# Performance work log

Measured on AMD Instinct MI355X. Metric: run time of the kernel, lower is better.

Reference implementation:

```python
import math
import jax, jax.numpy as jnp
import numpy as np
from jax import lax

B, C, H, W, D = 8, 3, 512, 512, 256
KS, SIGMA = 13, 2.0  # GaussianBlur(13); torchvision samples sigma in (0.1,5.0) -> fixed for determinism


def tanh01(v):
    return jnp.tanh(v) * 0.5 + 0.5


def tanh_range(v, left, right):
    return tanh01(v) * (right - left) + left


def norm01(v):
    return (v - v.min()) / (v.max() - v.min())


def gaussian_blur(x):
    r = KS // 2
    t = jnp.arange(KS, dtype=x.dtype) - r
    k = jnp.exp(-(t ** 2) / (2.0 * SIGMA ** 2))
    k = k / k.sum()
    b, c, h, w = x.shape
    xp = jnp.pad(x, ((0, 0), (0, 0), (r, r), (r, r)), mode='reflect').reshape(b * c, 1, h + 2 * r, w + 2 * r)
    y = lax.conv_general_dilated(xp, k.reshape(1, 1, KS, 1), (1, 1), 'VALID')
    y = lax.conv_general_dilated(y, k.reshape(1, 1, 1, KS), (1, 1), 'VALID')
    return y.reshape(b, c, h, w)


def dark_channel(x):
    return x.min(axis=1, keepdims=True)


def atmospheric_light(x, dark, top_k=1000):
    b, _, h, w = x.shape
    imsz = h * w
    numpx = max(imsz // top_k, 1)
    darkvec = dark.reshape(b, imsz)
    imvec = x.reshape(b, 3, imsz).transpose(0, 2, 1)  # [b, imsz, 3]
    idx = jnp.argsort(darkvec, axis=1)[:, imsz - numpx:]  # brightest dark-channel pixels
    gathered = jnp.take_along_axis(imvec, idx[:, :, None], axis=1)  # [b, numpx, 3]
    a = gathered[:, 1:, :].sum(axis=1) / numpx  # original loop skips index 0 of the slice
    return a[:, :, None, None]  # [b,3,1,1]


def fft_filter(x, rate, fft_gate):
    # rate: [b,1]; replicate torch.fft.fftshift default (shifts ALL axes, incl. batch/channel)
    b, c, w, h = x.shape  # note: original names w,h = shape[-2:]
    line = jnp.floor(jnp.sqrt(w * h * rate) / 2.0).astype(jnp.int32).reshape(-1)  # [b]
    rows = jnp.arange(w)
    cols = jnp.arange(h)
    mr = (rows[None, :] >= w // 2 - line[:, None]) & (rows[None, :] < w // 2 + line[:, None])
    mc = (cols[None, :] >= h // 2 - line[:, None]) & (cols[None, :] < h // 2 + line[:, None])
    mask = (mr[:, None, :, None] & mc[:, None, None, :]).astype(x.dtype)  # [b,1,w,h]
    mask = jnp.broadcast_to(mask, x.shape)
    F = jnp.fft.fftshift(jnp.fft.fft2(x, norm='forward'))
    F = F * (1.0 - mask)
    inv = jnp.fft.ifft2(jnp.fft.ifftshift(F), norm='forward').real
    return jnp.abs(inv) * fft_gate[:, None, None, None]


def setup_inputs() -> dict:
    key = jax.random.key(0)
    ks = jax.random.split(key, 20)
    def lin_w(k, i, o):
        return (jax.random.normal(k, (i, o)) * 0.02).astype(jnp.float32)
    def lin_b(k, o):
        return (jax.random.normal(k, (o,)) * 0.02).astype(jnp.float32)
    return {
        'x': jax.random.uniform(ks[0], (B, C, H, W), dtype=jnp.float32),
        'latent': (jax.random.normal(ks[1], (B, D)) * 0.5).astype(jnp.float32),
        'gate_w': lin_w(ks[2], D, 8), 'gate_b': lin_b(ks[3], 8),
        'wb_w': lin_w(ks[4], D, 3), 'wb_b': lin_b(ks[5], 3),
        'gamma_w': lin_w(ks[6], D, 1), 'gamma_b': lin_b(ks[7], 1),
        'sharp_w': lin_w(ks[8], D, 1), 'sharp_b': lin_b(ks[9], 1),
        'defog_w': lin_w(ks[10], D, 1), 'defog_b': lin_b(ks[11], 1),
        'contrast_w': lin_w(ks[12], D, 1), 'contrast_b': lin_b(ks[13], 1),
        'tone_w': lin_w(ks[14], D, 8), 'tone_b': lin_b(ks[15], 8),
        'fft_w': lin_w(ks[16], D, 1), 'fft_b': lin_b(ks[17], 1),
    }


def reference(x, latent, gate_w, gate_b, wb_w, wb_b, gamma_w, gamma_b, sharp_w, sharp_b,
              defog_w, defog_b, contrast_w, contrast_b, tone_w, tone_b, fft_w, fft_b):
    gate = tanh_range(latent @ gate_w + gate_b, 0.01, 1.0)  # [B,8]

    # white balance
    wb = jnp.exp(tanh_range(latent @ wb_w + wb_b, -0.5, 0.5))
    cs = 1.0 / (1e-5 + 0.27 * wb[:, 0] + 0.67 * wb[:, 1] + 0.06 * wb[:, 2])
    wb = cs[:, None] * wb
    wb_out = norm01(wb[:, :, None, None] * x) * gate[:, 0][:, None, None, None]

    # gamma balance
    lg = math.log(2.5)
    gamma = jnp.exp(tanh_range(latent @ gamma_w + gamma_b, -lg, lg))[:, :, None, None]
    g_out = norm01(jnp.maximum(x, 1e-4) ** gamma) * gate[:, 1][:, None, None, None]

    # identity
    id_out = x * gate[:, 2][:, None, None, None]

    # sharpening
    y = tanh_range(latent @ sharp_w + sharp_b, 0.1, 1.0)[:, :, None, None]
    s = x + y * (x - gaussian_blur(x))
    sharp_out = norm01(s) * gate[:, 3][:, None, None, None]

    # defog (atmospheric scattering model)
    omega = tanh_range(latent @ defog_w + defog_b, 0.1, 1.0)[:, :, None, None]
    dark = dark_channel(x)
    a = atmospheric_light(x, dark)
    t = 1.0 - omega * dark_channel(x / a)
    j = (x - a) / jnp.maximum(t, 0.01) + a
    fog_out = norm01(j) * gate[:, 4][:, None, None, None]

    # contrast
    alpha = jnp.tanh(latent @ contrast_w + contrast_b)[:, :, None, None]
    lum = jnp.clip(0.27 * x[:, 0] + 0.67 * x[:, 1] + 0.06 * x[:, 2], 0.0, 1.0)[:, None]
    clum = -jnp.cos(math.pi * lum) * 0.5 + 0.5
    cimg = x / (lum + 1e-6) * clum
    cimg = (1.0 - alpha) * x + alpha * cimg
    contrast_out = norm01(cimg) * gate[:, 5][:, None, None, None]

    # tone curve (8 fixed segments)
    tc = tanh_range(latent @ tone_w + tone_b, 0.5, 2.0)  # [B,8]
    tsum = tc.sum(axis=1) + 1e-30
    total = jnp.zeros_like(x)
    for i in range(8):
        total = total + jnp.clip(x - i / 8.0, 0.0, 1.0 / 8.0) * tc[:, i][:, None, None, None]
    total = total * (8.0 / tsum)[:, None, None, None]
    tone_out = norm01(total) * gate[:, 6][:, None, None, None]

    # fft frequency masking
    rate = tanh_range(latent @ fft_w + fft_b, 0.1, 0.8)  # [B,1]
    fft_out = fft_filter(x, rate, gate[:, 7])

    return norm01(wb_out + g_out + id_out + sharp_out + fog_out + contrast_out + tone_out + fft_out)
```

## Files before the change

kernel.cpp:

```cpp
#include <hip/hip_runtime.h>
#include <math.h>

#define HW 262144
#define TOTAL 6291456
#define PI_F 3.14159265358979323846f
#define NBIN 1024
#define PIDX(i) ((i) + ((i) >> 3))


#define PF_GATE 0
#define PF_WB 64
#define PF_GAMMA 88
#define PF_Y 96
#define PF_OMEGA 104
#define PF_ALPHA 112
#define PF_TC 120
#define PF_TSC 184
#define PF_RATE 192
#define PF_FG 200
#define PF_A 208
#define PF_WBM 256
#define PF_WBA 264
#define PF_GM 272
#define PF_GA 280
#define PF_SM 288
#define PF_SA 296
#define PF_FM 304
#define PF_FA 312
#define PF_CM 320
#define PF_CA 328
#define PF_TM 336
#define PF_TA 344
#define PF_LINE 360

#define QX(b,c) ((b)*3+(c))
#define QS 24
#define QJ 25
#define QC 26
#define QFIN 27
#define SL_LCOUNT 1792
#define SL_BINSTAR 1920
#define SL_RNEED 1928
#define SL_SUMA2 2048

struct GK { float w[13]; };

__device__ __forceinline__ unsigned fkey(float f){
    unsigned u = __float_as_uint(f);
    return (u & 0x80000000u) ? ~u : (u | 0x80000000u);
}
__device__ __forceinline__ float funkey(unsigned k){
    return (k & 0x80000000u) ? __uint_as_float(k & 0x7FFFFFFFu) : __uint_as_float(~k);
}

__device__ __forceinline__ void blockRedPair(unsigned kmn, unsigned kmx, int q,
                                             unsigned* slots, unsigned* lds8){
    #pragma unroll
    for (int o = 32; o > 0; o >>= 1){
        kmn = min(kmn, __shfl_down(kmn, o));
        kmx = max(kmx, __shfl_down(kmx, o));
    }
    int w = threadIdx.x >> 6;
    if ((threadIdx.x & 63) == 0){ lds8[w] = kmn; lds8[4+w] = kmx; }
    __syncthreads();
    if (threadIdx.x == 0){
        unsigned mn = min(min(lds8[0],lds8[1]), min(lds8[2],lds8[3]));
        unsigned mx = max(max(lds8[4],lds8[5]), max(lds8[6],lds8[7]));
        int s = blockIdx.x & 31;
        atomicMin(&slots[q*64 + s], mn);
        atomicMax(&slots[q*64 + 32 + s], mx);
    }
    __syncthreads();
}

__device__ __forceinline__ float toneF(float v, const float* tc, float tsc){
    float tn = 0.f;
    #pragma unroll
    for (int i = 0; i < 8; ++i){
        float d = v - 0.125f * (float)i;
        d = fminf(fmaxf(d, 0.f), 0.125f);
        tn += d * tc[i];
    }
    return tn * tsc;
}

__device__ __forceinline__ float2 cadd(float2 a, float2 b){ return make_float2(a.x+b.x, a.y+b.y); }
__device__ __forceinline__ float2 csub(float2 a, float2 b){ return make_float2(a.x-b.x, a.y-b.y); }
__device__ __forceinline__ float2 cmul(float2 a, float2 b){ return make_float2(a.x*b.x - a.y*b.y, a.x*b.y + a.y*b.x); }

template<int S>
__device__ __forceinline__ float2 rot90(float2 z){
    return (S < 0) ? make_float2(z.y, -z.x) : make_float2(-z.y, z.x);
}

template<int S>
__device__ __forceinline__ void fft4p(float2 a, float2 b, float2 c, float2 d,
                                      float2& X0, float2& X1, float2& X2, float2& X3){
    float2 t0 = cadd(a,c), t1 = csub(a,c), t2 = cadd(b,d), t3 = csub(b,d);
    float2 it3 = rot90<S>(t3);
    X0 = cadd(t0,t2); X2 = csub(t0,t2);
    X1 = cadd(t1,it3); X3 = csub(t1,it3);
}

template<int S>
__device__ __forceinline__ void bfly8(float2 v[8]){
    const float C = 0.70710678118654752f;
    float2 E0,E1,E2,E3,O0,O1,O2,O3;
    fft4p<S>(v[0],v[2],v[4],v[6], E0,E1,E2,E3);
    fft4p<S>(v[1],v[3],v[5],v[7], O0,O1,O2,O3);
    float2 w1 = make_float2(C, (S<0) ? -C : C);
    float2 w3 = make_float2(-C, (S<0) ? -C : C);
    float2 u1 = cmul(O1, w1);
    float2 u2 = rot90<S>(O2);
    float2 u3 = cmul(O3, w3);
    v[0]=cadd(E0,O0); v[4]=csub(E0,O0);
    v[1]=cadd(E1,u1); v[5]=csub(E1,u1);
    v[2]=cadd(E2,u2); v[6]=csub(E2,u2);
    v[3]=cadd(E3,u3); v[7]=csub(E3,u3);
}

__device__ __forceinline__ void twiddles(float2 v[8], float th){
    float sn, cs; __sincosf(th, &sn, &cs);
    float2 w1 = make_float2(cs, sn);
    float2 w = w1;
    v[1] = cmul(v[1], w1);
    #pragma unroll
    for (int r = 2; r < 8; ++r){ w = cmul(w, w1); v[r] = cmul(v[r], w); }
}

template<int S>
__device__ __forceinline__ void fft512reg(float2 v[8], float2* buf, int lane){
    bfly8<S>(v);
    #pragma unroll
    for (int q = 0; q < 8; ++q) buf[PIDX(8*lane + q)] = v[q];
    __syncthreads();
    #pragma unroll
    for (int r = 0; r < 8; ++r) v[r] = buf[PIDX(lane + 64*r)];
    __syncthreads();
    twiddles(v, (float)S * 6.2831853072f * (float)(lane & 7) * (1.0f/64.0f));
    bfly8<S>(v);
    {
        int basei = ((lane >> 3) << 6) + (lane & 7);
        #pragma unroll
        for (int q = 0; q < 8; ++q) buf[PIDX(basei + 8*q)] = v[q];
    }
    __syncthreads();
    #pragma unroll
    for (int r = 0; r < 8; ++r) v[r] = buf[PIDX(lane + 64*r)];
    twiddles(v, (float)S * 6.2831853072f * (float)lane * (1.0f/512.0f));
    bfly8<S>(v);
}

__global__ __launch_bounds__(256) void kSetup(
    const float* __restrict__ lat,
    const float* gw, const float* gb, const float* wbw, const float* wbb,
    const float* gaw, const float* gab, const float* shw, const float* shb,
    const float* dfw, const float* dfb, const float* ctw, const float* ctb,
    const float* tow, const float* tob, const float* ffw, const float* ffb,
    float* P, unsigned* slots, unsigned* hist)
{
    if (blockIdx.x != 0){
        int i = (blockIdx.x - 1) * 256 + threadIdx.x;
        if (i < 4096) slots[i] = (i < 1792 && (i & 63) < 32) ? 0xFFFFFFFFu : 0u;
        if (i < 8192) hist[i] = 0u;
        return;
    }
    int t = threadIdx.x;
    if (t < 192){
        int b = t / 24, o = t % 24;
        const float* L = lat + b * 256;
        const float* W; float bias; int nc, col;
        if (o < 8)      { W=gw;  bias=gb[o];     nc=8; col=o;    }
        else if (o < 11){ W=wbw; bias=wbb[o-8];  nc=3; col=o-8;  }
        else if (o==11) { W=gaw; bias=gab[0];    nc=1; col=0;    }
        else if (o==12) { W=shw; bias=shb[0];    nc=1; col=0;    }
        else if (o==13) { W=dfw; bias=dfb[0];    nc=1; col=0;    }
        else if (o==14) { W=ctw; bias=ctb[0];    nc=1; col=0;    }
        else if (o<23)  { W=tow; bias=tob[o-15]; nc=8; col=o-15; }
        else            { W=ffw; bias=ffb[0];    nc=1; col=0;    }
        float acc = bias;
        for (int d = 0; d < 256; ++d) acc += L[d] * W[d*nc + col];
        float t01 = tanhf(acc) * 0.5f + 0.5f;
        if (o < 8){ float v = t01*0.99f + 0.01f; P[PF_GATE + b*8 + o] = v; if (o==7) P[PF_FG + b] = v; }
        else if (o < 11){ P[PF_WB + b*3 + (o-8)] = expf(t01 - 0.5f); }
        else if (o==11){ float lg = logf(2.5f); P[PF_GAMMA + b] = expf(t01*(2.f*lg) - lg); }
        else if (o==12){ P[PF_Y + b] = t01*0.9f + 0.1f; }
        else if (o==13){ P[PF_OMEGA + b] = t01*0.9f + 0.1f; }
        else if (o==14){ P[PF_ALPHA + b] = tanhf(acc); }
        else if (o<23){ P[PF_TC + b*8 + (o-15)] = t01*1.5f + 0.5f; }
        else { P[PF_RATE + b] = t01*0.7f + 0.1f; }
    }
    __syncthreads();
    if (t < 8){
        int b = t;
        float w0=P[PF_WB+b*3], w1=P[PF_WB+b*3+1], w2=P[PF_WB+b*3+2];
        float cs = 1.0f / (1e-5f + 0.27f*w0 + 0.67f*w1 + 0.06f*w2);
        P[PF_WB+b*3] = cs*w0; P[PF_WB+b*3+1] = cs*w1; P[PF_WB+b*3+2] = cs*w2;
        float ts = 0.f;
        for (int i = 0; i < 8; ++i) ts += P[PF_TC + b*8 + i];
        P[PF_TSC + b] = 8.0f / (ts + 1e-30f);
        int bs = (b + 4) & 7;
        ((int*)(P + PF_LINE))[b] = (int)floorf(sqrtf(262144.0f * P[PF_RATE + bs]) * 0.5f);
    }
}

__global__ __launch_bounds__(256) void kMinmaxHist(const float* __restrict__ x, unsigned* slots, unsigned* hist){
    __shared__ unsigned h[NBIN];
    __shared__ unsigned lds8[8];
    int b = blockIdx.x >> 7;
    int blk = blockIdx.x & 127;
    for (int i = threadIdx.x; i < NBIN; i += 256) h[i] = 0u;
    __syncthreads();
    size_t xb = (size_t)b*3*HW;
    int p0 = (((blk<<1)    )*256 + threadIdx.x) << 2;
    int p1 = (((blk<<1) + 1)*256 + threadIdx.x) << 2;
    float4 u0 = *(const float4*)(x + xb + p0);
    float4 u1 = *(const float4*)(x + xb + HW + p0);
    float4 u2 = *(const float4*)(x + xb + 2*HW + p0);
    float4 w0 = *(const float4*)(x + xb + p1);
    float4 w1 = *(const float4*)(x + xb + HW + p1);
    float4 w2 = *(const float4*)(x + xb + 2*HW + p1);
    float a0[8] = {u0.x,u0.y,u0.z,u0.w, w0.x,w0.y,w0.z,w0.w};
    float a1[8] = {u1.x,u1.y,u1.z,u1.w, w1.x,w1.y,w1.z,w1.w};
    float a2[8] = {u2.x,u2.y,u2.z,u2.w, w2.x,w2.y,w2.z,w2.w};
    float mn0=1e30f,mx0=-1e30f,mn1=1e30f,mx1=-1e30f,mn2=1e30f,mx2=-1e30f;
    #pragma unroll
    for (int e = 0; e < 8; ++e){
        float dark = fminf(a0[e], fminf(a1[e], a2[e]));
        atomicAdd(&h[min(NBIN-1, (int)(dark * (float)NBIN))], 1u);
        mn0 = fminf(mn0, a0[e]); mx0 = fmaxf(mx0, a0[e]);
        mn1 = fminf(mn1, a1[e]); mx1 = fmaxf(mx1, a1[e]);
        mn2 = fminf(mn2, a2[e]); mx2 = fmaxf(mx2, a2[e]);
    }
    __syncthreads();
    for (int i = threadIdx.x; i < NBIN; i += 256){
        unsigned c = h[i];
        if (c) atomicAdd(&hist[b*NBIN + i], c);
    }
    blockRedPair(fkey(mn0), fkey(mx0), QX(b,0), slots, lds8);
    blockRedPair(fkey(mn1), fkey(mx1), QX(b,1), slots, lds8);
    blockRedPair(fkey(mn2), fkey(mx2), QX(b,2), slots, lds8);
}

__global__ __launch_bounds__(256) void kScanHist(const unsigned* __restrict__ hist, unsigned* slots){
    int b = blockIdx.x, t = threadIdx.x;
    __shared__ unsigned wtot[4];
    __shared__ int doneS;
    if (t == 0) doneS = 0;
    __syncthreads();
    unsigned total = 0;
    for (int c0 = 0; c0 < NBIN; c0 += 256){
        int binIdx = NBIN-1 - (c0 + t);
        unsigned cnt = hist[b*NBIN + binIdx];
        unsigned v = cnt;
        #pragma unroll
        for (int off = 1; off < 64; off <<= 1){
            unsigned u = __shfl_up(v, off);
            if ((t & 63) >= off) v += u;
        }
        if ((t & 63) == 63) wtot[t >> 6] = v;
        __syncthreads();
        unsigned wofs = 0;
        for (int w = 0; w < (t >> 6); ++w) wofs += wtot[w];
        unsigned incl = total + wofs + v;
        unsigned excl = incl - cnt;
        if (incl >= 261u && excl < 261u){
            slots[SL_BINSTAR + b] = (unsigned)binIdx;
            slots[SL_RNEED + b]   = 261u - excl;
            doneS = 1;
        }
        __syncthreads();
        if (doneS) break;
        total += wtot[0] + wtot[1] + wtot[2] + wtot[3];
        __syncthreads();
    }
}

__global__ __launch_bounds__(256) void kCollect(const float* __restrict__ x, unsigned* slots, uint2* list){
    __shared__ float wsum[3][4];
    int b = blockIdx.x >> 8;
    int tile = blockIdx.x & 255;
    size_t xb = (size_t)b*3*HW;
    int p = (tile*256 + threadIdx.x) << 2;
    float4 v0 = *(const float4*)(x + xb + p);
    float4 v1 = *(const float4*)(x + xb + HW + p);
    float4 v2 = *(const float4*)(x + xb + 2*HW + p);
    int bs = (int)slots[SL_BINSTAR + b];
    float a0[4] = {v0.x,v0.y,v0.z,v0.w};
    float a1[4] = {v1.x,v1.y,v1.z,v1.w};
    float a2[4] = {v2.x,v2.y,v2.z,v2.w};
    float s0 = 0.f, s1 = 0.f, s2 = 0.f;
    #pragma unroll
    for (int e = 0; e < 4; ++e){
        float dark = fminf(a0[e], fminf(a1[e], a2[e]));
        int bin = min(NBIN-1, (int)(dark * (float)NBIN));
        if (bin > bs){ s0 += a0[e]; s1 += a1[e]; s2 += a2[e]; }
        else if (bin == bs){
            unsigned n = atomicAdd(&slots[SL_LCOUNT + b], 1u);
            if (n < 1024u) list[(b << 10) + n] = make_uint2(__float_as_uint(dark), (unsigned)(p + e));
        }
    }
    #pragma unroll
    for (int o = 32; o > 0; o >>= 1){
        s0 += __shfl_down(s0, o); s1 += __shfl_down(s1, o); s2 += __shfl_down(s2, o);
    }
    int w = threadIdx.x >> 6;
    if ((threadIdx.x & 63) == 0){ wsum[0][w] = s0; wsum[1][w] = s1; wsum[2][w] = s2; }
    __syncthreads();
    if (threadIdx.x == 0){
        float t0 = wsum[0][0]+wsum[0][1]+wsum[0][2]+wsum[0][3];
        float t1 = wsum[1][0]+wsum[1][1]+wsum[1][2]+wsum[1][3];
        float t2 = wsum[2][0]+wsum[2][1]+wsum[2][2]+wsum[2][3];
        float* F = (float*)(slots + SL_SUMA2);
        int sl = blockIdx.x & 31;
        atomicAdd(&F[(b*3+0)*32 + sl], t0);
        atomicAdd(&F[(b*3+1)*32 + sl], t1);
        atomicAdd(&F[(b*3+2)*32 + sl], t2);
    }
}

__global__ void kSelect(const float* __restrict__ x, uint2* list, unsigned* slots, float* P){
    __shared__ unsigned pid[262];
    __shared__ char taken[1024];
    int b = blockIdx.x, t = threadIdx.x;
    int n = (int)min(slots[SL_LCOUNT + b], 1024u);
    int r = (int)slots[SL_RNEED + b];
    if (r > n) r = n;
    const uint2* L = &list[b << 10];
    for (int i = t; i < n; i += 64) taken[i] = 0;
    __syncthreads();
    for (int it = 0; it < r; ++it){
        unsigned long long bk = 0ull; int bp = -1;
        for (int i = t; i < n; i += 64){
            if (taken[i]) continue;
            uint2 e = L[i];
            unsigned long long key = ((unsigned long long)e.x << 32) | e.y;
            if (key > bk){ bk = key; bp = i; }
        }
        #pragma unroll
        for (int o = 32; o > 0; o >>= 1){
            unsigned long long ok = __shfl_down(bk, o);
            int op = __shfl_down(bp, o);
            if (ok > bk){ bk = ok; bp = op; }
        }
        bp = __shfl(bp, 0);
        if (t == 0){ pid[it] = L[bp].y; taken[bp] = 1; }
        __syncthreads();
    }
    float s0 = 0.f, s1 = 0.f, s2 = 0.f;
    size_t xb = (size_t)b*3*HW;
    for (int i = t; i < r; i += 64){
        unsigned id = pid[i];
        s0 += x[xb + id]; s1 += x[xb + HW + id]; s2 += x[xb + 2*HW + id];
    }
    #pragma unroll
    for (int o = 32; o > 0; o >>= 1){
        s0 += __shfl_down(s0, o); s1 += __shfl_down(s1, o); s2 += __shfl_down(s2, o);
    }
    if (t == 0){
        const float* F = (const float*)(slots + SL_SUMA2);
        float f0 = 0.f, f1 = 0.f, f2 = 0.f;
        for (int k = 0; k < 32; ++k){
            f0 += F[(b*3+0)*32 + k];
            f1 += F[(b*3+1)*32 + k];
            f2 += F[(b*3+2)*32 + k];
        }
        P[PF_A + b*3+0] = (s0 + f0) / 262.0f;
        P[PF_A + b*3+1] = (s1 + f1) / 262.0f;
        P[PF_A + b*3+2] = (s2 + f2) / 262.0f;
    }
}

__global__ __launch_bounds__(256) void kBlur(const float* __restrict__ x, float* __restrict__ blurOut,
                                             const float* __restrict__ P, unsigned* slots, GK gk){
    __shared__ float tile[76][80];
    __shared__ float hbuf[76][68];
    __shared__ unsigned lds8[8];
    int img = blockIdx.x >> 6;
    int tid = blockIdx.x & 63;
    int tr0 = (tid >> 3) << 6;
    int tc0 = (tid & 7) << 6;
    size_t ib = (size_t)img * HW;
    int t = threadIdx.x;
    for (int l = t; l < 76*76; l += 256){
        int r = l / 76, c = l - r*76;
        int gr = tr0 + r - 6; gr = (gr < 0) ? -gr : ((gr > 511) ? 1022 - gr : gr);
        int gc = tc0 + c - 6; gc = (gc < 0) ? -gc : ((gc > 511) ? 1022 - gc : gc);
        tile[r][c] = x[ib + ((size_t)gr << 9) + gc];
    }
    __syncthreads();
    for (int l = t; l < 76*64; l += 256){
        int r = l >> 6, c = l & 63;
        float acc = 0.f;
        #pragma unroll
        for (int k = 0; k < 13; ++k) acc += gk.w[k] * tile[r][c + k];
        hbuf[r][c] = acc;
    }
    __syncthreads();
    float yb = P[PF_Y + img/3];
    unsigned kmn = 0xFFFFFFFFu, kmx = 0u;
    for (int l = t; l < 64*64; l += 256){
        int r = l >> 6, c = l & 63;
        float acc = 0.f;
        #pragma unroll
        for (int k = 0; k < 13; ++k) acc += gk.w[k] * hbuf[r + k][c];
        blurOut[ib + ((size_t)(tr0 + r) << 9) + tc0 + c] = acc;
        float xv = tile[r + 6][c + 6];
        float s = xv + yb * (xv - acc);
        unsigned key = fkey(s);
        kmn = min(kmn, key); kmx = max(kmx, key);
    }
    blockRedPair(kmn, kmx, QS, slots, lds8);
}

__global__ __launch_bounds__(256) void kFftRowFwdJC(const float* __restrict__ x, float2* __restrict__ bc,
                                                    const float* __restrict__ P, unsigned* slots){
    __shared__ float xs[3][512];
    __shared__ float2 buf[3][580];
    __shared__ unsigned lds8[8];
    int b = blockIdx.x >> 9;
    int row = blockIdx.x & 511;
    int t = threadIdx.x;
    size_t rowoff = ((size_t)row << 9);
    #pragma unroll
    for (int ch = 0; ch < 3; ++ch){
        float2 z = *(const float2*)(x + (size_t)(3*b + ch)*HW + rowoff + 2*t);
        xs[ch][2*t] = z.x; xs[ch][2*t+1] = z.y;
    }
    __syncthreads();
    {
        float a0 = P[PF_A+b*3], a1 = P[PF_A+b*3+1], a2 = P[PF_A+b*3+2];
        float om = P[PF_OMEGA+b], al = P[PF_ALPHA+b];
        float jmn = 1e30f, jmx = -1e30f, cmn = 1e30f, cmx = -1e30f;
        #pragma unroll
        for (int e = 0; e < 2; ++e){
            int i = 2*t + e;
            float x0 = xs[0][i], x1 = xs[1][i], x2 = xs[2][i];
            float dr = fminf(x0/a0, fminf(x1/a1, x2/a2));
            float T = fmaxf(1.0f - om*dr, 0.01f);
            float j0 = (x0-a0)/T + a0, j1 = (x1-a1)/T + a1, j2 = (x2-a2)/T + a2;
            float lum = fminf(fmaxf(0.27f*x0 + 0.67f*x1 + 0.06f*x2, 0.f), 1.f);
            float clum = -__cosf(PI_F*lum)*0.5f + 0.5f;
            float il = clum / (lum + 1e-6f);
            float c0 = (1.f-al)*x0 + al*(x0*il);
            float c1 = (1.f-al)*x1 + al*(x1*il);
            float c2 = (1.f-al)*x2 + al*(x2*il);
            jmn = fminf(jmn, fminf(j0, fminf(j1, j2))); jmx = fmaxf(jmx, fmaxf(j0, fmaxf(j1, j2)));
            cmn = fminf(cmn, fminf(c0, fminf(c1, c2))); cmx = fmaxf(cmx, fmaxf(c0, fmaxf(c1, c2)));
        }
        blockRedPair(fkey(jmn), fkey(jmx), QJ, slots, lds8);
        blockRedPair(fkey(cmn), fkey(cmx), QC, slots, lds8);
    }
    bool act = t < 192;
    int ch = t >> 6, lane = t & 63;
    float2 v[8];
    if (act){
        #pragma unroll
        for (int r = 0; r < 8; ++r) v[r] = make_float2(xs[ch][lane + 64*r] * (1.0f/512.0f), 0.f);
        bfly8<-1>(v);
        #pragma unroll
        for (int q = 0; q < 8; ++q) buf[ch][PIDX(8*lane + q)] = v[q];
    }
    __syncthreads();
    if (act){
        #pragma unroll
        for (int r = 0; r < 8; ++r) v[r] = buf[ch][PIDX(lane + 64*r)];
    }
    __syncthreads();
    if (act){
        twiddles(v, -6.2831853072f * (float)(lane & 7) * (1.0f/64.0f));
        bfly8<-1>(v);
        int basei = ((lane >> 3) << 6) + (lane & 7);
        #pragma unroll
        for (int q = 0; q < 8; ++q) buf[ch][PIDX(basei + 8*q)] = v[q];
    }
    __syncthreads();
    if (act){
        #pragma unroll
        for (int r = 0; r < 8; ++r) v[r] = buf[ch][PIDX(lane + 64*r)];
        twiddles(v, -6.2831853072f * (float)lane * (1.0f/512.0f));
        bfly8<-1>(v);
        size_t ib = (size_t)(3*b + ch)*HW + rowoff;
        #pragma unroll
        for (int q = 0; q < 8; ++q) bc[ib + lane + 64*q] = v[q];
    }
}

__global__ __launch_bounds__(256) void kFftColMid(float2* __restrict__ bc, const int* __restrict__ lineS){
    int img  = blockIdx.x >> 6;
    int tile = blockIdx.x & 63;
    int c0 = tile << 3;
    int line = lineS[img / 3];
    if (c0 >= line && c0 + 8 <= 512 - line) return;
    __shared__ float2 cb[8][580];
    int t = threadIdx.x;
    size_t ibase = (size_t)img*HW + c0;
    for (int k = 0; k < 16; ++k){
        int idx = (k << 8) + t;
        int row = idx >> 3, col = idx & 7;
        float2 z = bc[ibase + ((size_t)row << 9) + col];
        cb[col][PIDX(row)] = make_float2(z.x * (1.0f/512.0f), z.y * (1.0f/512.0f));
    }
    __syncthreads();
    int lane = t & 63;
    #pragma unroll
    for (int h = 0; h < 2; ++h){
        int col = (h << 2) + (t >> 6);
        int cc = c0 + col;
        bool colM = (cc < line) || (cc >= 512 - line);
        float2 v[8];
        #pragma unroll
        for (int r = 0; r < 8; ++r) v[r] = cb[col][PIDX(lane + 64*r)];
        __syncthreads();
        fft512reg<-1>(v, cb[col], lane);
        if (colM){
            #pragma unroll
            for (int q = 0; q < 8; ++q){
                int f = lane + (q << 6);
                if (f < line || f >= 512 - line) v[q] = make_float2(0.f, 0.f);
            }
        }
        __syncthreads();
        fft512reg<+1>(v, cb[col], lane);
        __syncthreads();
        #pragma unroll
        for (int q = 0; q < 8; ++q) cb[col][PIDX(lane + 64*q)] = v[q];
        __syncthreads();
    }
    for (int k = 0; k < 16; ++k){
        int idx = (k << 8) + t;
        int row = idx >> 3, col = idx & 7;
        int cc = c0 + col;
        if (cc < line || cc >= 512 - line)
            bc[ibase + ((size_t)row << 9) + col] = cb[col][PIDX(row)];
    }
}

__global__ __launch_bounds__(256) void kCombineFFT(const float* __restrict__ x, float* __restrict__ outb,
                                                   const float2* __restrict__ bc, const float* __restrict__ P,
                                                   unsigned* slots){
    __shared__ float2 buf[3][580];
    __shared__ float fbuf[3][512];
    __shared__ unsigned lds8[8];
    int b = blockIdx.x >> 9;
    int row = blockIdx.x & 511;
    int t = threadIdx.x;
    bool act = t < 192;
    int ch = t >> 6, lane = t & 63;
    size_t rowoff = ((size_t)row << 9);
    float2 v[8];
    if (act){
        size_t ib = (size_t)(3*b + ch)*HW + rowoff;
        #pragma unroll
        for (int r = 0; r < 8; ++r) v[r] = bc[ib + lane + 64*r];
        bfly8<1>(v);
        #pragma unroll
        for (int q = 0; q < 8; ++q) buf[ch][PIDX(8*lane + q)] = v[q];
    }
    __syncthreads();
    if (act){
        #pragma unroll
        for (int r = 0; r < 8; ++r) v[r] = buf[ch][PIDX(lane + 64*r)];
    }
    __syncthreads();
    if (act){
        twiddles(v, 6.2831853072f * (float)(lane & 7) * (1.0f/64.0f));
        bfly8<1>(v);
        int basei = ((lane >> 3) << 6) + (lane & 7);
        #pragma unroll
        for (int q = 0; q < 8; ++q) buf[ch][PIDX(basei + 8*q)] = v[q];
    }
    __syncthreads();
    if (act){
        #pragma unroll
        for (int r = 0; r < 8; ++r) v[r] = buf[ch][PIDX(lane + 64*r)];
        twiddles(v, 6.2831853072f * (float)lane * (1.0f/512.0f));
        bfly8<1>(v);
        #pragma unroll
        for (int q = 0; q < 8; ++q) fbuf[ch][lane + 64*q] = fabsf(v[q].x);
    }
    __syncthreads();

    float g  = P[PF_FG + b];
    float wb0=P[PF_WB+b*3], wb1=P[PF_WB+b*3+1], wb2=P[PF_WB+b*3+2];
    float gam=P[PF_GAMMA+b], yb=P[PF_Y+b], om=P[PF_OMEGA+b], al=P[PF_ALPHA+b];
    float a0=P[PF_A+b*3], a1=P[PF_A+b*3+1], a2=P[PF_A+b*3+2];
    float g2=P[PF_GATE+b*8+2];
    float wbm=P[PF_WBM+b], wba=P[PF_WBA+b], gm=P[PF_GM+b], ga=P[PF_GA+b];
    float sm=P[PF_SM+b], sa=P[PF_SA+b], fm=P[PF_FM+b], fa=P[PF_FA+b];
    float cm=P[PF_CM+b], ca=P[PF_CA+b], tm=P[PF_TM+b], ta=P[PF_TA+b];
    float tc[8];
    #pragma unroll
    for (int i = 0; i < 8; ++i) tc[i] = P[PF_TC + b*8 + i];
    float tsc = P[PF_TSC+b];

    size_t p0 = (size_t)(3*b)*HW + rowoff + 2*t;
    float2 xv0 = *(const float2*)(x + p0);
    float2 xv1 = *(const float2*)(x + p0 + HW);
    float2 xv2 = *(const float2*)(x + p0 + 2*HW);
    float2 bv0 = *(const float2*)(outb + p0);
    float2 bv1 = *(const float2*)(outb + p0 + HW);
    float2 bv2 = *(const float2*)(outb + p0 + 2*HW);
    float X0[2] = {xv0.x, xv0.y}, X1[2] = {xv1.x, xv1.y}, X2[2] = {xv2.x, xv2.y};
    float B0[2] = {bv0.x, bv0.y}, B1[2] = {bv1.x, bv1.y}, B2[2] = {bv2.x, bv2.y};
    float O0[2], O1[2], O2[2];
    float mn = 1e30f, mx = -1e30f;
    #pragma unroll
    for (int e = 0; e < 2; ++e){
        int i = 2*t + e;
        float f0 = fbuf[0][i] * g;
        float f1 = fbuf[1][i] * g;
        float f2 = fbuf[2][i] * g;
        float x0 = X0[e], x1 = X1[e], x2 = X2[e];
        float dr = fminf(x0/a0, fminf(x1/a1, x2/a2));
        float T = fmaxf(1.0f - om*dr, 0.01f);
        float lum = fminf(fmaxf(0.27f*x0 + 0.67f*x1 + 0.06f*x2, 0.f), 1.f);
        float clum = -__cosf(PI_F*lum)*0.5f + 0.5f;
        float il = clum / (lum + 1e-6f);
        float s, j, ci, tn, gp;
        s = x0 + yb*(x0 - B0[e]); j = (x0 - a0)/T + a0; ci = (1.f-al)*x0 + al*(x0*il);
        tn = toneF(x0, tc, tsc); gp = __powf(fmaxf(x0, 1e-4f), gam);
        float sum0 = (wb0*x0)*wbm + wba + gp*gm + ga + x0*g2 + s*sm + sa + j*fm + fa + ci*cm + ca + tn*tm + ta + f0;
        s = x1 + yb*(x1 - B1[e]); j = (x1 - a1)/T + a1; ci = (1.f-al)*x1 + al*(x1*il);
        tn = toneF(x1, tc, tsc); gp = __powf(fmaxf(x1, 1e-4f), gam);
        float sum1 = (wb1*x1)*wbm + wba + gp*gm + ga + x1*g2 + s*sm + sa + j*fm + fa + ci*cm + ca + tn*tm + ta + f1;
        s = x2 + yb*(x2 - B2[e]); j = (x2 - a2)/T + a2; ci = (1.f-al)*x2 + al*(x2*il);
        tn = toneF(x2, tc, tsc); gp = __powf(fmaxf(x2, 1e-4f), gam);
        float sum2 = (wb2*x2)*wbm + wba + gp*gm + ga + x2*g2 + s*sm + sa + j*fm + fa + ci*cm + ca + tn*tm + ta + f2;
        O0[e] = sum0; O1[e] = sum1; O2[e] = sum2;
        mn = fminf(mn, fminf(sum0, fminf(sum1, sum2)));
        mx = fmaxf(mx, fmaxf(sum0, fmaxf(sum1, sum2)));
    }
    *(float2*)(outb + p0)        = make_float2(O0[0], O0[1]);
    *(float2*)(outb + p0 + HW)   = make_float2(O1[0], O1[1]);
    *(float2*)(outb + p0 + 2*HW) = make_float2(O2[0], O2[1]);
    blockRedPair(fkey(mn), fkey(mx), QFIN, slots, lds8);
}

__global__ void kNormParams(float* P, const unsigned* __restrict__ slots){
    __shared__ float mnv[28], mxv[28];
    int t = threadIdx.x;
    if (t < 28){
        unsigned kmn = 0xFFFFFFFFu, kmx = 0u;
        for (int s = 0; s < 32; ++s){
            kmn = min(kmn, slots[t*64 + s]);
            kmx = max(kmx, slots[t*64 + 32 + s]);
        }
        mnv[t] = funkey(kmn); mxv[t] = funkey(kmx);
    }
    __syncthreads();
    if (t == 0){
        float wmin=1e30f, wmax=-1e30f, gmin=1e30f, gmax=-1e30f, tmin=1e30f, tmax=-1e30f;
        for (int b = 0; b < 8; ++b){
            float gam = P[PF_GAMMA+b];
            float tsc = P[PF_TSC+b];
            const float* tc = &P[PF_TC + b*8];
            float xbmin = 1e30f, xbmax = -1e30f;
            for (int c = 0; c < 3; ++c){
                int i = b*3 + c;
                float w = P[PF_WB + i];
                wmin = fminf(wmin, w * mnv[i]); wmax = fmaxf(wmax, w * mxv[i]);
                gmin = fminf(gmin, __powf(fmaxf(mnv[i], 1e-4f), gam));
                gmax = fmaxf(gmax, __powf(fmaxf(mxv[i], 1e-4f), gam));
                xbmin = fminf(xbmin, mnv[i]); xbmax = fmaxf(xbmax, mxv[i]);
            }
            tmin = fminf(tmin, toneF(xbmin, tc, tsc));
            tmax = fmaxf(tmax, toneF(xbmax, tc, tsc));
        }
        float smin = mnv[QS], smax = mxv[QS];
        float jmin = mnv[QJ], jmax = mxv[QJ];
        float cmin = mnv[QC], cmax = mxv[QC];
        for (int b = 0; b < 8; ++b){
            const float* G = &P[PF_GATE + b*8];
            float m;
            m = G[0]/(wmax-wmin); P[PF_WBM+b]=m; P[PF_WBA+b]=-wmin*m;
            m = G[1]/(gmax-gmin); P[PF_GM +b]=m; P[PF_GA +b]=-gmin*m;
            m = G[3]/(smax-smin); P[PF_SM +b]=m; P[PF_SA +b]=-smin*m;
            m = G[4]/(jmax-jmin); P[PF_FM +b]=m; P[PF_FA +b]=-jmin*m;
            m = G[5]/(cmax-cmin); P[PF_CM +b]=m; P[PF_CA +b]=-cmin*m;
            m = G[6]/(tmax-tmin); P[PF_TM +b]=m; P[PF_TA +b]=-tmin*m;
        }
    }
}

__global__ __launch_bounds__(256) void kFinalNorm(float* __restrict__ out, const unsigned* __restrict__ slots){
    unsigned kmn = 0xFFFFFFFFu, kmx = 0u;
    for (int s = 0; s < 32; ++s){
        kmn = min(kmn, slots[QFIN*64 + s]);
        kmx = max(kmx, slots[QFIN*64 + 32 + s]);
    }
    float mn = funkey(kmn), mx = funkey(kmx);
    float inv = 1.0f / (mx - mn);
    size_t i = ((size_t)blockIdx.x*256 + threadIdx.x) << 2;
    float4 v = *(const float4*)(out + i);
    v.x = (v.x - mn) * inv; v.y = (v.y - mn) * inv;
    v.z = (v.z - mn) * inv; v.w = (v.w - mn) * inv;
    *(float4*)(out + i) = v;
}

extern "C" void kernel_launch(void* const* d_in, const int* in_sizes, int n_in,
                              void* d_out, int out_size, void* d_ws, size_t ws_size,
                              hipStream_t stream){
    const float* x   = (const float*)d_in[0];
    const float* lat = (const float*)d_in[1];
    const float* gw  = (const float*)d_in[2];  const float* gb  = (const float*)d_in[3];
    const float* wbw = (const float*)d_in[4];  const float* wbb = (const float*)d_in[5];
    const float* gaw = (const float*)d_in[6];  const float* gab = (const float*)d_in[7];
    const float* shw = (const float*)d_in[8];  const float* shb = (const float*)d_in[9];
    const float* dfw = (const float*)d_in[10]; const float* dfb = (const float*)d_in[11];
    const float* ctw = (const float*)d_in[12]; const float* ctb = (const float*)d_in[13];
    const float* tow = (const float*)d_in[14]; const float* tob = (const float*)d_in[15];
    const float* ffw = (const float*)d_in[16]; const float* ffb = (const float*)d_in[17];
    float* out = (float*)d_out;
    char* ws = (char*)d_ws;

    float*    P     = (float*)ws;
    unsigned* slots = (unsigned*)(ws + 2048);
    unsigned* hist  = (unsigned*)(ws + 20480);
    uint2*    list  = (uint2*)(ws + 540672);
    float2*   bufC  = (float2*)(ws + 1048576);
    const int* lineS = (const int*)(P + PF_LINE);

    GK gk;
    {
        float s = 0.f;
        for (int i = 0; i < 13; ++i){ float t = (float)i - 6.f; gk.w[i] = expf(-(t*t)/8.0f); s += gk.w[i]; }
        for (int i = 0; i < 13; ++i) gk.w[i] /= s;
    }

    hipLaunchKernelGGL(kSetup,       dim3(41),   dim3(256), 0, stream, lat, gw,gb,wbw,wbb,gaw,gab,shw,shb,dfw,dfb,ctw,ctb,tow,tob,ffw,ffb, P, slots, hist);
    hipLaunchKernelGGL(kMinmaxHist,  dim3(1024), dim3(256), 0, stream, x, slots, hist);
    hipLaunchKernelGGL(kScanHist,    dim3(8),    dim3(256), 0, stream, hist, slots);
    hipLaunchKernelGGL(kCollect,     dim3(2048), dim3(256), 0, stream, x, slots, list);
    hipLaunchKernelGGL(kSelect,      dim3(8),    dim3(64),  0, stream, x, list, slots, P);
    hipLaunchKernelGGL(kBlur,        dim3(1536), dim3(256), 0, stream, x, out, P, slots, gk);
    hipLaunchKernelGGL(kFftRowFwdJC, dim3(4096), dim3(256), 0, stream, x, bufC, P, slots);
    hipLaunchKernelGGL(kFftColMid,   dim3(1536), dim3(256), 0, stream, bufC, lineS);
    hipLaunchKernelGGL(kNormParams,  dim3(1),    dim3(64),  0, stream, P, slots);
    hipLaunchKernelGGL(kCombineFFT,  dim3(4096), dim3(256), 0, stream, x, out, bufC, P, slots);
    hipLaunchKernelGGL(kFinalNorm,   dim3(6144), dim3(256), 0, stream, out, slots);
}
```

Before: 236.7 us.

## Pack two real channels per complex FFT and process two rows per block

Channels R and G are packed into one complex signal (R + iG), and B goes into a second one. The row FFTs, the column pass and the inverse row FFTs then run on 2 complex images per batch instead of 3. Each block now handles two rows with all 256 threads active and float4 loads. Divisions by the atmospheric light are replaced with precomputed reciprocals, and the 8-segment tone curve becomes a single table lookup using precomputed prefix sums. Packing is only correct if the frequency mask is conjugate-symmetric, and the lookup changes floating-point rounding slightly.

```diff
diff --git a/kernel.cpp b/kernel.cpp
--- a/kernel.cpp
+++ b/kernel.cpp
@@ -32,6 +32,9 @@
 #define PF_TM 336
 #define PF_TA 344
 #define PF_LINE 360
+#define PF_TCS 368
+#define PF_TPRE 432
+#define PF_IA 496
 
 #define QX(b,c) ((b)*3+(c))
 #define QS 24
@@ -198,7 +201,15 @@
         P[PF_WB+b*3] = cs*w0; P[PF_WB+b*3+1] = cs*w1; P[PF_WB+b*3+2] = cs*w2;
         float ts = 0.f;
         for (int i = 0; i < 8; ++i) ts += P[PF_TC + b*8 + i];
-        P[PF_TSC + b] = 8.0f / (ts + 1e-30f);
+        float tsc = 8.0f / (ts + 1e-30f);
+        P[PF_TSC + b] = tsc;
+        float acc = 0.f;
+        for (int k = 0; k < 8; ++k){
+            float tck = P[PF_TC + b*8 + k] * tsc;
+            P[PF_TCS + b*8 + k] = tck;
+            P[PF_TPRE + b*8 + k] = acc;
+            acc += tck * 0.125f;
+        }
         int bs = (b + 4) & 7;
         ((int*)(P + PF_LINE))[b] = (int)floorf(sqrtf(262144.0f * P[PF_RATE + bs]) * 0.5f);
     }
@@ -365,9 +376,9 @@
             f1 += F[(b*3+1)*32 + k];
             f2 += F[(b*3+2)*32 + k];
         }
-        P[PF_A + b*3+0] = (s0 + f0) / 262.0f;
-        P[PF_A + b*3+1] = (s1 + f1) / 262.0f;
-        P[PF_A + b*3+2] = (s2 + f2) / 262.0f;
+        float A0 = (s0 + f0) / 262.0f, A1 = (s1 + f1) / 262.0f, A2 = (s2 + f2) / 262.0f;
+        P[PF_A + b*3+0] = A0; P[PF_A + b*3+1] = A1; P[PF_A + b*3+2] = A2;
+        P[PF_IA + b*3+0] = 1.0f/A0; P[PF_IA + b*3+1] = 1.0f/A1; P[PF_IA + b*3+2] = 1.0f/A2;
     }
 }
 
@@ -415,82 +426,69 @@
 
 __global__ __launch_bounds__(256) void kFftRowFwdJC(const float* __restrict__ x, float2* __restrict__ bc,
                                                     const float* __restrict__ P, unsigned* slots){
-    __shared__ float xs[3][512];
-    __shared__ float2 buf[3][580];
+    __shared__ float xs[2][3][512];
+    __shared__ float2 buf[4][580];
     __shared__ unsigned lds8[8];
-    int b = blockIdx.x >> 9;
-    int row = blockIdx.x & 511;
+    int b = blockIdx.x >> 8;
+    int rp = blockIdx.x & 255;
     int t = threadIdx.x;
-    size_t rowoff = ((size_t)row << 9);
-    #pragma unroll
-    for (int ch = 0; ch < 3; ++ch){
-        float2 z = *(const float2*)(x + (size_t)(3*b + ch)*HW + rowoff + 2*t);
-        xs[ch][2*t] = z.x; xs[ch][2*t+1] = z.y;
+    #pragma unroll
+    for (int k = 0; k < 3; ++k){
+        int l = t + (k << 8);
+        int seg = l >> 7;
+        int idx = (l & 127) << 2;
+        int ch = seg >> 1, rr = seg & 1;
+        float4 z = *(const float4*)(x + (size_t)(3*b + ch)*HW + ((size_t)(2*rp + rr) << 9) + idx);
+        *(float4*)&xs[rr][ch][idx] = z;
     }
     __syncthreads();
     {
-        float a0 = P[PF_A+b*3], a1 = P[PF_A+b*3+1], a2 = P[PF_A+b*3+2];
+        float ia0 = P[PF_IA+b*3], ia1 = P[PF_IA+b*3+1], ia2 = P[PF_IA+b*3+2];
+        float a0 = P[PF_A+b*3],  a1 = P[PF_A+b*3+1],  a2 = P[PF_A+b*3+2];
         float om = P[PF_OMEGA+b], al = P[PF_ALPHA+b];
+        int rr = t >> 7, c4 = (t & 127) << 2;
+        float4 xv0 = *(float4*)&xs[rr][0][c4];
+        float4 xv1 = *(float4*)&xs[rr][1][c4];
+        float4 xv2 = *(float4*)&xs[rr][2][c4];
+        float A0[4]={xv0.x,xv0.y,xv0.z,xv0.w}, A1[4]={xv1.x,xv1.y,xv1.z,xv1.w}, A2[4]={xv2.x,xv2.y,xv2.z,xv2.w};
         float jmn = 1e30f, jmx = -1e30f, cmn = 1e30f, cmx = -1e30f;
         #pragma unroll
-        for (int e = 0; e < 2; ++e){
-            int i = 2*t + e;
-            float x0 = xs[0][i], x1 = xs[1][i], x2 = xs[2][i];
-            float dr = fminf(x0/a0, fminf(x1/a1, x2/a2));
+        for (int e = 0; e < 4; ++e){
+            float x0 = A0[e], x1 = A1[e], x2 = A2[e];
+            float dr = fminf(x0*ia0, fminf(x1*ia1, x2*ia2));
             float T = fmaxf(1.0f - om*dr, 0.01f);
-            float j0 = (x0-a0)/T + a0, j1 = (x1-a1)/T + a1, j2 = (x2-a2)/T + a2;
+            float rT = 1.0f / T;
+            float j0 = (x0-a0)*rT + a0, j1 = (x1-a1)*rT + a1, j2 = (x2-a2)*rT + a2;
             float lum = fminf(fmaxf(0.27f*x0 + 0.67f*x1 + 0.06f*x2, 0.f), 1.f);
             float clum = -__cosf(PI_F*lum)*0.5f + 0.5f;
-            float il = clum / (lum + 1e-6f);
-            float c0 = (1.f-al)*x0 + al*(x0*il);
-            float c1 = (1.f-al)*x1 + al*(x1*il);
-            float c2 = (1.f-al)*x2 + al*(x2*il);
+            float alx = (1.f - al) + al * (clum / (lum + 1e-6f));
+            float c0 = x0*alx, c1 = x1*alx, c2 = x2*alx;
             jmn = fminf(jmn, fminf(j0, fminf(j1, j2))); jmx = fmaxf(jmx, fmaxf(j0, fmaxf(j1, j2)));
             cmn = fminf(cmn, fminf(c0, fminf(c1, c2))); cmx = fmaxf(cmx, fmaxf(c0, fmaxf(c1, c2)));
         }
         blockRedPair(fkey(jmn), fkey(jmx), QJ, slots, lds8);
         blockRedPair(fkey(cmn), fkey(cmx), QC, slots, lds8);
     }
-    bool act = t < 192;
-    int ch = t >> 6, lane = t & 63;
+    int u = t >> 6, lane = t & 63;
+    int frr = u >> 1, pk = u & 1;
     float2 v[8];
-    if (act){
-        #pragma unroll
-        for (int r = 0; r < 8; ++r) v[r] = make_float2(xs[ch][lane + 64*r] * (1.0f/512.0f), 0.f);
-        bfly8<-1>(v);
-        #pragma unroll
-        for (int q = 0; q < 8; ++q) buf[ch][PIDX(8*lane + q)] = v[q];
-    }
-    __syncthreads();
-    if (act){
-        #pragma unroll
-        for (int r = 0; r < 8; ++r) v[r] = buf[ch][PIDX(lane + 64*r)];
-    }
-    __syncthreads();
-    if (act){
-        twiddles(v, -6.2831853072f * (float)(lane & 7) * (1.0f/64.0f));
-        bfly8<-1>(v);
-        int basei = ((lane >> 3) << 6) + (lane & 7);
-        #pragma unroll
-        for (int q = 0; q < 8; ++q) buf[ch][PIDX(basei + 8*q)] = v[q];
-    }
-    __syncthreads();
-    if (act){
-        #pragma unroll
-        for (int r = 0; r < 8; ++r) v[r] = buf[ch][PIDX(lane + 64*r)];
-        twiddles(v, -6.2831853072f * (float)lane * (1.0f/512.0f));
-        bfly8<-1>(v);
-        size_t ib = (size_t)(3*b + ch)*HW + rowoff;
-        #pragma unroll
-        for (int q = 0; q < 8; ++q) bc[ib + lane + 64*q] = v[q];
-    }
+    #pragma unroll
+    for (int r = 0; r < 8; ++r){
+        int i = lane + 64*r;
+        if (pk == 0) v[r] = make_float2(xs[frr][0][i] * (1.0f/512.0f), xs[frr][1][i] * (1.0f/512.0f));
+        else         v[r] = make_float2(xs[frr][2][i] * (1.0f/512.0f), 0.f);
+    }
+    fft512reg<-1>(v, buf[u], lane);
+    size_t ob = (size_t)(2*b + pk)*HW + ((size_t)(2*rp + frr) << 9);
+    #pragma unroll
+    for (int q = 0; q < 8; ++q) bc[ob + lane + 64*q] = v[q];
 }
 
 __global__ __launch_bounds__(256) void kFftColMid(float2* __restrict__ bc, const int* __restrict__ lineS){
     int img  = blockIdx.x >> 6;
     int tile = blockIdx.x & 63;
     int c0 = tile << 3;
-    int line = lineS[img / 3];
+    int line = lineS[img >> 1];
     if (c0 >= line && c0 + 8 <= 512 - line) return;
     __shared__ float2 cb[8][580];
     int t = threadIdx.x;
@@ -539,45 +537,31 @@
 __global__ __launch_bounds__(256) void kCombineFFT(const float* __restrict__ x, float* __restrict__ outb,
                                                    const float2* __restrict__ bc, const float* __restrict__ P,
                                                    unsigned* slots){
-    __shared__ float2 buf[3][580];
-    __shared__ float fbuf[3][512];
+    __shared__ float2 buf[4][580];
+    __shared__ float fbuf[2][3][512];
+    __shared__ float stc[8], spre[8];
     __shared__ unsigned lds8[8];
-    int b = blockIdx.x >> 9;
-    int row = blockIdx.x & 511;
+    int b = blockIdx.x >> 8;
+    int rp = blockIdx.x & 255;
     int t = threadIdx.x;
-    bool act = t < 192;
-    int ch = t >> 6, lane = t & 63;
-    size_t rowoff = ((size_t)row << 9);
+    if (t < 8){ stc[t] = P[PF_TCS + b*8 + t]; spre[t] = P[PF_TPRE + b*8 + t]; }
+    int u = t >> 6, lane = t & 63;
+    int frr = u >> 1, pk = u & 1;
     float2 v[8];
-    if (act){
-        size_t ib = (size_t)(3*b + ch)*HW + rowoff;
-        #pragma unroll
-        for (int r = 0; r < 8; ++r) v[r] = bc[ib + lane + 64*r];
-        bfly8<1>(v);
-        #pragma unroll
-        for (int q = 0; q < 8; ++q) buf[ch][PIDX(8*lane + q)] = v[q];
-    }
-    __syncthreads();
-    if (act){
-        #pragma unroll
-        for (int r = 0; r < 8; ++r) v[r] = buf[ch][PIDX(lane + 64*r)];
-    }
-    __syncthreads();
-    if (act){
-        twiddles(v, 6.2831853072f * (float)(lane & 7) * (1.0f/64.0f));
-        bfly8<1>(v);
-        int basei = ((lane >> 3) << 6) + (lane & 7);
-        #pragma unroll
-        for (int q = 0; q < 8; ++q) buf[ch][PIDX(basei + 8*q)] = v[q];
-    }
-    __syncthreads();
-    if (act){
-        #pragma unroll
-        for (int r = 0; r < 8; ++r) v[r] = buf[ch][PIDX(lane + 64*r)];
-        twiddles(v, 6.2831853072f * (float)lane * (1.0f/512.0f));
-        bfly8<1>(v);
-        #pragma unroll
-        for (int q = 0; q < 8; ++q) fbuf[ch][lane + 64*q] = fabsf(v[q].x);
+    size_t ib = (size_t)(2*b + pk)*HW + ((size_t)(2*rp + frr) << 9);
+    #pragma unroll
+    for (int r = 0; r < 8; ++r) v[r] = bc[ib + lane + 64*r];
+    fft512reg<+1>(v, buf[u], lane);
+    if (pk == 0){
+        #pragma unroll
+        for (int q = 0; q < 8; ++q){
+            int i = lane + 64*q;
+            fbuf[frr][0][i] = fabsf(v[q].x);
+            fbuf[frr][1][i] = fabsf(v[q].y);
+        }
+    } else {
+        #pragma unroll
+        for (int q = 0; q < 8; ++q) fbuf[frr][2][lane + 64*q] = fabsf(v[q].x);
     }
     __syncthreads();
 
@@ -585,55 +569,59 @@
     float wb0=P[PF_WB+b*3], wb1=P[PF_WB+b*3+1], wb2=P[PF_WB+b*3+2];
     float gam=P[PF_GAMMA+b], yb=P[PF_Y+b], om=P[PF_OMEGA+b], al=P[PF_ALPHA+b];
     float a0=P[PF_A+b*3], a1=P[PF_A+b*3+1], a2=P[PF_A+b*3+2];
+    float ia0=P[PF_IA+b*3], ia1=P[PF_IA+b*3+1], ia2=P[PF_IA+b*3+2];
     float g2=P[PF_GATE+b*8+2];
     float wbm=P[PF_WBM+b], wba=P[PF_WBA+b], gm=P[PF_GM+b], ga=P[PF_GA+b];
     float sm=P[PF_SM+b], sa=P[PF_SA+b], fm=P[PF_FM+b], fa=P[PF_FA+b];
     float cm=P[PF_CM+b], ca=P[PF_CA+b], tm=P[PF_TM+b], ta=P[PF_TA+b];
-    float tc[8];
-    #pragma unroll
-    for (int i = 0; i < 8; ++i) tc[i] = P[PF_TC + b*8 + i];
-    float tsc = P[PF_TSC+b];
-
-    size_t p0 = (size_t)(3*b)*HW + rowoff + 2*t;
-    float2 xv0 = *(const float2*)(x + p0);
-    float2 xv1 = *(const float2*)(x + p0 + HW);
-    float2 xv2 = *(const float2*)(x + p0 + 2*HW);
-    float2 bv0 = *(const float2*)(outb + p0);
-    float2 bv1 = *(const float2*)(outb + p0 + HW);
-    float2 bv2 = *(const float2*)(outb + p0 + 2*HW);
-    float X0[2] = {xv0.x, xv0.y}, X1[2] = {xv1.x, xv1.y}, X2[2] = {xv2.x, xv2.y};
-    float B0[2] = {bv0.x, bv0.y}, B1[2] = {bv1.x, bv1.y}, B2[2] = {bv2.x, bv2.y};
-    float O0[2], O1[2], O2[2];
+    float kadd = wba + ga + sa + fa + ca + ta;
+
+    int rr = t >> 7, c4 = (t & 127) << 2;
+    size_t p0 = (size_t)(3*b)*HW + ((size_t)(2*rp + rr) << 9) + c4;
+    float4 xv0 = *(const float4*)(x + p0);
+    float4 xv1 = *(const float4*)(x + p0 + HW);
+    float4 xv2 = *(const float4*)(x + p0 + 2*HW);
+    float4 bv0 = *(const float4*)(outb + p0);
+    float4 bv1 = *(const float4*)(outb + p0 + HW);
+    float4 bv2 = *(const float4*)(outb + p0 + 2*HW);
+    float4 fv0 = *(float4*)&fbuf[rr][0][c4];
+    float4 fv1 = *(float4*)&fbuf[rr][1][c4];
+    float4 fv2 = *(float4*)&fbuf[rr][2][c4];
+    float X0[4]={xv0.x,xv0.y,xv0.z,xv0.w}, X1[4]={xv1.x,xv1.y,xv1.z,xv1.w}, X2[4]={xv2.x,xv2.y,xv2.z,xv2.w};
+    float B0[4]={bv0.x,bv0.y,bv0.z,bv0.w}, B1[4]={bv1.x,bv1.y,bv1.z,bv1.w}, B2[4]={bv2.x,bv2.y,bv2.z,bv2.w};
+    float F0[4]={fv0.x,fv0.y,fv0.z,fv0.w}, F1[4]={fv1.x,fv1.y,fv1.z,fv1.w}, F2[4]={fv2.x,fv2.y,fv2.z,fv2.w};
+    float O0[4], O1[4], O2[4];
     float mn = 1e30f, mx = -1e30f;
     #pragma unroll
-    for (int e = 0; e < 2; ++e){
-        int i = 2*t + e;
-        float f0 = fbuf[0][i] * g;
-        float f1 = fbuf[1][i] * g;
-        float f2 = fbuf[2][i] * g;
+    for (int e = 0; e < 4; ++e){
         float x0 = X0[e], x1 = X1[e], x2 = X2[e];
-        float dr = fminf(x0/a0, fminf(x1/a1, x2/a2));
+        float dr = fminf(x0*ia0, fminf(x1*ia1, x2*ia2));
         float T = fmaxf(1.0f - om*dr, 0.01f);
+        float rT = 1.0f / T;
         float lum = fminf(fmaxf(0.27f*x0 + 0.67f*x1 + 0.06f*x2, 0.f), 1.f);
         float clum = -__cosf(PI_F*lum)*0.5f + 0.5f;
-        float il = clum / (lum + 1e-6f);
-        float s, j, ci, tn, gp;
-        s = x0 + yb*(x0 - B0[e]); j = (x0 - a0)/T + a0; ci = (1.f-al)*x0 + al*(x0*il);
-        tn = toneF(x0, tc, tsc); gp = __powf(fmaxf(x0, 1e-4f), gam);
-        float sum0 = (wb0*x0)*wbm + wba + gp*gm + ga + x0*g2 + s*sm + sa + j*fm + fa + ci*cm + ca + tn*tm + ta + f0;
-        s = x1 + yb*(x1 - B1[e]); j = (x1 - a1)/T + a1; ci = (1.f-al)*x1 + al*(x1*il);
-        tn = toneF(x1, tc, tsc); gp = __powf(fmaxf(x1, 1e-4f), gam);
-        float sum1 = (wb1*x1)*wbm + wba + gp*gm + ga + x1*g2 + s*sm + sa + j*fm + fa + ci*cm + ca + tn*tm + ta + f1;
-        s = x2 + yb*(x2 - B2[e]); j = (x2 - a2)/T + a2; ci = (1.f-al)*x2 + al*(x2*il);
-        tn = toneF(x2, tc, tsc); gp = __powf(fmaxf(x2, 1e-4f), gam);
-        float sum2 = (wb2*x2)*wbm + wba + gp*gm + ga + x2*g2 + s*sm + sa + j*fm + fa + ci*cm + ca + tn*tm + ta + f2;
-        O0[e] = sum0; O1[e] = sum1; O2[e] = sum2;
-        mn = fminf(mn, fminf(sum0, fminf(sum1, sum2)));
-        mx = fmaxf(mx, fmaxf(sum0, fmaxf(sum1, sum2)));
-    }
-    *(float2*)(outb + p0)        = make_float2(O0[0], O0[1]);
-    *(float2*)(outb + p0 + HW)   = make_float2(O1[0], O1[1]);
-    *(float2*)(outb + p0 + 2*HW) = make_float2(O2[0], O2[1]);
+        float alx = (1.f - al) + al * (clum / (lum + 1e-6f));
+        #pragma unroll
+        for (int ch = 0; ch < 3; ++ch){
+            float xv = (ch==0)?x0:((ch==1)?x1:x2);
+            float bl = (ch==0)?B0[e]:((ch==1)?B1[e]:B2[e]);
+            float fv = (ch==0)?F0[e]:((ch==1)?F1[e]:F2[e]);
+            float wb = (ch==0)?wb0:((ch==1)?wb1:wb2);
+            float av = (ch==0)?a0:((ch==1)?a1:a2);
+            float s = xv + yb*(xv - bl);
+            float j = (xv - av)*rT + av;
+            float ci = xv * alx;
+            int k = min(7, (int)(xv * 8.0f));
+            float tn = spre[k] + (xv - 0.125f*(float)k) * stc[k];
+            float gp = __powf(fmaxf(xv, 1e-4f), gam);
+            float sum = (wb*xv)*wbm + gp*gm + xv*g2 + s*sm + j*fm + ci*cm + tn*tm + kadd + fv*g;
+            if (ch==0) O0[e]=sum; else if (ch==1) O1[e]=sum; else O2[e]=sum;
+            mn = fminf(mn, sum); mx = fmaxf(mx, sum);
+        }
+    }
+    *(float4*)(outb + p0)        = make_float4(O0[0],O0[1],O0[2],O0[3]);
+    *(float4*)(outb + p0 + HW)   = make_float4(O1[0],O1[1],O1[2],O1[3]);
+    *(float4*)(outb + p0 + 2*HW) = make_float4(O2[0],O2[1],O2[2],O2[3]);
     blockRedPair(fkey(mn), fkey(mx), QFIN, slots, lds8);
 }
 
@@ -715,7 +703,7 @@
     char* ws = (char*)d_ws;
 
     float*    P     = (float*)ws;
-    unsigned* slots = (unsigned*)(ws + 2048);
+    unsigned* slots = (unsigned*)(ws + 4096);
     unsigned* hist  = (unsigned*)(ws + 20480);
     uint2*    list  = (uint2*)(ws + 540672);
     float2*   bufC  = (float2*)(ws + 1048576);
@@ -734,9 +722,9 @@
     hipLaunchKernelGGL(kCollect,     dim3(2048), dim3(256), 0, stream, x, slots, list);
     hipLaunchKernelGGL(kSelect,      dim3(8),    dim3(64),  0, stream, x, list, slots, P);
     hipLaunchKernelGGL(kBlur,        dim3(1536), dim3(256), 0, stream, x, out, P, slots, gk);
-    hipLaunchKernelGGL(kFftRowFwdJC, dim3(4096), dim3(256), 0, stream, x, bufC, P, slots);
-    hipLaunchKernelGGL(kFftColMid,   dim3(1536), dim3(256), 0, stream, bufC, lineS);
+    hipLaunchKernelGGL(kFftRowFwdJC, dim3(2048), dim3(256), 0, stream, x, bufC, P, slots);
+    hipLaunchKernelGGL(kFftColMid,   dim3(1024), dim3(256), 0, stream, bufC, lineS);
     hipLaunchKernelGGL(kNormParams,  dim3(1),    dim3(64),  0, stream, P, slots);
-    hipLaunchKernelGGL(kCombineFFT,  dim3(4096), dim3(256), 0, stream, x, out, bufC, P, slots);
+    hipLaunchKernelGGL(kCombineFFT,  dim3(2048), dim3(256), 0, stream, x, out, bufC, P, slots);
     hipLaunchKernelGGL(kFinalNorm,   dim3(6144), dim3(256), 0, stream, out, slots);
 }
```

Measured after the change: 204.1 us. 13.7% less time.
